# Optimization experiments

Measured on AMD Instinct MI355X. Metric: run time of the kernel, lower is better.

## Reference

```python
import jax, jax.numpy as jnp
import numpy as np

SEQ, B, IN_DIM, EMB, HID, L = 2048, 32, 512, 256, 256, 16
START, STOP = 0, 1
HH = HID // 2  # per-direction hidden size
NEG = -10000.0


def _lstm_dir(xs, Wih, Whh, b, h0, c0, reverse):
    # xs: (T, B, EMB); Wih: (4*HH, EMB); Whh: (4*HH, HH); b: (4*HH,)
    def step(carry, x):
        h, c = carry
        g = x @ Wih.T + h @ Whh.T + b  # (B, 4*HH)
        i, f, gg, o = jnp.split(g, 4, axis=-1)  # PyTorch gate order i,f,g,o
        c = jax.nn.sigmoid(f) * c + jax.nn.sigmoid(i) * jnp.tanh(gg)
        h = jax.nn.sigmoid(o) * jnp.tanh(c)
        return (h, c), h
    _, hs = jax.lax.scan(step, (h0, c0), xs, reverse=reverse)
    return hs  # (T, B, HH)


def _features(source_seq, in_W, in_b, Wih_f, Whh_f, b_f, Wih_b, Whh_b, b_b,
              out_W, out_b, h0, c0):
    x = source_seq @ in_W.T + in_b  # (T, B, EMB)
    hf = _lstm_dir(x, Wih_f, Whh_f, b_f, h0[0], c0[0], reverse=False)
    hb = _lstm_dir(x, Wih_b, Whh_b, b_b, h0[1], c0[1], reverse=True)
    h = jnp.concatenate([hf, hb], axis=-1)  # (T, B, HID)
    return h @ out_W.T + out_b  # (T, B, L)


def _viterbi(feats, transitions):
    # transitions[i, j]: score of transitioning to label i from label j
    fv = jnp.full((B, L), NEG, feats.dtype).at[:, START].set(0.0)

    def step(fv, feat):
        scores = fv[:, None, :] + transitions[None, :, :]  # (B, next, prev)
        bp = jnp.argmax(scores, axis=2).astype(jnp.int32)   # (B, L)
        fv = jnp.max(scores, axis=2) + feat
        return fv, bp

    fv, bps = jax.lax.scan(step, fv, feats)  # bps: (T, B, L)
    term = fv + transitions[STOP][None, :]   # (B, L)
    score = jnp.max(term, axis=1)            # (B,)
    best_last = jnp.argmax(term, axis=1).astype(jnp.int32)  # (B,)

    def back(lbl, bp):
        prev = jnp.take_along_axis(bp, lbl[:, None], axis=1)[:, 0]
        return prev, lbl

    _, path = jax.lax.scan(back, best_last, bps, reverse=True)  # (T, B)
    return score, path


def setup_inputs() -> dict:
    key = jax.random.key(0)
    ks = jax.random.split(key, 16)
    s = 0.05
    return {
        "source_seq": jax.random.normal(ks[0], (SEQ, B, IN_DIM), jnp.float32),
        "in_W": jax.random.normal(ks[1], (EMB, IN_DIM), jnp.float32) * s,
        "in_b": jnp.zeros((EMB,), jnp.float32),
        "Wih_f": jax.random.normal(ks[2], (4 * HH, EMB), jnp.float32) * s,
        "Whh_f": jax.random.normal(ks[3], (4 * HH, HH), jnp.float32) * s,
        "b_f": jnp.zeros((4 * HH,), jnp.float32),
        "Wih_b": jax.random.normal(ks[4], (4 * HH, EMB), jnp.float32) * s,
        "Whh_b": jax.random.normal(ks[5], (4 * HH, HH), jnp.float32) * s,
        "b_b": jnp.zeros((4 * HH,), jnp.float32),
        "out_W": jax.random.normal(ks[6], (L, HID), jnp.float32) * s,
        "out_b": jnp.zeros((L,), jnp.float32),
        "transitions": jax.random.normal(ks[7], (L, L), jnp.float32),
        "h0": jax.random.normal(ks[8], (2, B, HH), jnp.float32),
        "c0": jax.random.normal(ks[9], (2, B, HH), jnp.float32),
    }


def reference(source_seq, in_W, in_b, Wih_f, Whh_f, b_f, Wih_b, Whh_b, b_b,
              out_W, out_b, transitions, h0, c0):
    feats = _features(source_seq, in_W, in_b, Wih_f, Whh_f, b_f,
                      Wih_b, Whh_b, b_b, out_W, out_b, h0, c0)
    score, labels = _viterbi(feats, transitions)
    return score, labels
```

## Files before the change

kernel.cpp:

```cpp
#include <hip/hip_runtime.h>
#include <hip/hip_bf16.h>

typedef __attribute__((ext_vector_type(8))) short bf16x8;
typedef __attribute__((ext_vector_type(4))) float f32x4;
typedef __attribute__((ext_vector_type(4))) unsigned u32x4;
typedef __attribute__((ext_vector_type(2))) unsigned u32x2;

#define SEQT 2048
#define BATCH 32
#define INDIM 512
#define EMB 256
#define HHX 128
#define LBL 16
#define LOG2E 1.44269504f

__device__ __forceinline__ unsigned short f2bf(float f) {
    unsigned u = __float_as_uint(f);
    u += 0x7FFFu + ((u >> 16) & 1u);
    return (unsigned short)(u >> 16);
}
#define BLO(u) __uint_as_float((u) << 16)
#define BHI(u) __uint_as_float((u) & 0xffff0000u)

__device__ __forceinline__ float cell(float ig, float fg, float gg, float og, float& c) {
    float Ef = __builtin_amdgcn_exp2f(fminf(fg, 30.f));
    float Ei = __builtin_amdgcn_exp2f(fminf(ig, 30.f));
    float Eg = __builtin_amdgcn_exp2f(fminf(gg, 60.f));
    float Eo = __builtin_amdgcn_exp2f(fminf(og, 30.f));
    float pf = 1.f + Ef;
    float t1 = (Eg + 1.f) * (1.f + Ei);
    float num = c * t1 + (Eg - 1.f) * pf;
    float cn = num * __builtin_amdgcn_rcpf(pf * t1);
    c = cn;
    float E2 = __builtin_amdgcn_exp2f(fminf(2.f * LOG2E * cn, 60.f));
    float r3 = __builtin_amdgcn_rcpf((E2 + 1.f) * (1.f + Eo));
    return (E2 - 1.f) * r3;
}

__device__ __forceinline__ int orig_of(int gp) {
    return ((gp >> 4) & 3) * 128 + (gp >> 6) * 16 + (gp & 15);
}
__device__ __forceinline__ float gate_scale(int gp) {
    return (((gp >> 4) & 3) == 2) ? (2.f * LOG2E) : (-LOG2E);
}

__global__ __launch_bounds__(256) void k_prep_wc(
    const float* __restrict__ in_W, const float* __restrict__ in_b,
    const float* __restrict__ Wih_f, const float* __restrict__ b_f,
    const float* __restrict__ Wih_b, const float* __restrict__ b_b,
    unsigned short* __restrict__ Wc, float* __restrict__ bc)
{
    int G0 = blockIdx.x * 8;
    int tid = threadIdx.x;
    __shared__ float wrow[8][EMB];
    for (int e = tid; e < 8 * EMB; e += 256) {
        int r = e >> 8, ee = e & 255;
        int G = G0 + r, dir = G >> 9, gp = G & 511;
        wrow[r][ee] = (dir ? Wih_b : Wih_f)[orig_of(gp) * EMB + ee] * gate_scale(gp);
    }
    __syncthreads();
    for (int k = tid; k < INDIM; k += 256) {
        float acc[8] = {0, 0, 0, 0, 0, 0, 0, 0};
        #pragma unroll 4
        for (int e = 0; e < EMB; ++e) {
            float x = in_W[e * INDIM + k];
            #pragma unroll
            for (int r = 0; r < 8; ++r) acc[r] += wrow[r][e] * x;
        }
        #pragma unroll
        for (int r = 0; r < 8; ++r) Wc[(size_t)(G0 + r) * INDIM + k] = f2bf(acc[r]);
    }
    if (tid < 64) {
        for (int r = 0; r < 8; ++r) {
            float p = 0.f;
            for (int e = tid; e < EMB; e += 64) p += wrow[r][e] * in_b[e];
            for (int off = 32; off; off >>= 1) p += __shfl_xor(p, off);
            if (tid == 0) {
                int G = G0 + r, dir = G >> 9, gp = G & 511;
                bc[G] = (dir ? b_b : b_f)[orig_of(gp)] * gate_scale(gp) + p;
            }
        }
    }
}

__global__ __launch_bounds__(256) void k_prep_misc(
    const float* __restrict__ Whh_f, const float* __restrict__ Whh_b,
    const float* __restrict__ out_W,
    unsigned short* __restrict__ Whh_bf, unsigned short* __restrict__ outW_bf)
{
    int idx = blockIdx.x * 256 + threadIdx.x;
    int stride = gridDim.x * 256;
    for (int i = idx; i < 1024 * HHX; i += stride) {
        int G = i >> 7, k = i & 127;
        int dir = G >> 9, gp = G & 511;
        const float* Whh = dir ? Whh_b : Whh_f;
        Whh_bf[i] = f2bf(Whh[orig_of(gp) * HHX + k] * gate_scale(gp));
    }
    for (int i = idx; i < LBL * 256; i += stride) outW_bf[i] = f2bf(out_W[i]);
}

__global__ __launch_bounds__(512) void k_gemm_p(
    const float* __restrict__ S, const unsigned short* __restrict__ Wc,
    const float* __restrict__ bc, unsigned short* __restrict__ P2)
{
    int m0 = blockIdx.y * 64;
    int n0 = blockIdx.x * 256;
    int tid = threadIdx.x;
    int w = tid >> 6, l = tid & 63;
    int lr = l & 15, lq = l >> 4;
    int wm = w >> 2, wn = w & 3;

    __shared__ __align__(16) unsigned short Alds[64 * 64];
    __shared__ __align__(16) unsigned short Blds[256 * 64];

    const f32x4 fzero = {0.f, 0.f, 0.f, 0.f};
    f32x4 acc[2][4];
    #pragma unroll
    for (int a = 0; a < 2; ++a)
        #pragma unroll
        for (int b = 0; b < 4; ++b) acc[a][b] = fzero;

    for (int kt = 0; kt < 8; ++kt) {
        {
            int r = tid >> 3, c = tid & 7;
            const float* src = S + (size_t)(m0 + r) * INDIM + kt * 64 + c * 8;
            float4 v0 = *(const float4*)src;
            float4 v1 = *(const float4*)(src + 4);
            unsigned g0, g1, g2, g3;
            asm("v_cvt_pk_bf16_f32 %0, %1, %2" : "=v"(g0) : "v"(v0.x), "v"(v0.y));
            asm("v_cvt_pk_bf16_f32 %0, %1, %2" : "=v"(g1) : "v"(v0.z), "v"(v0.w));
            asm("v_cvt_pk_bf16_f32 %0, %1, %2" : "=v"(g2) : "v"(v1.x), "v"(v1.y));
            asm("v_cvt_pk_bf16_f32 %0, %1, %2" : "=v"(g3) : "v"(v1.z), "v"(v1.w));
            u32x4 wv = {g0, g1, g2, g3};
            *(u32x4*)((char*)Alds + r * 128 + ((c * 16) ^ ((r & 7) << 4))) = wv;
        }
        {
            int r = tid >> 1, h = tid & 1;
            const unsigned short* bs = Wc + (size_t)(n0 + r) * INDIM + kt * 64;
            #pragma unroll
            for (int cc = 0; cc < 4; ++cc) {
                int ch = h * 4 + cc;
                bf16x8 v = *(const bf16x8*)(bs + ch * 8);
                *(bf16x8*)((char*)Blds + r * 128 + ((ch * 16) ^ ((r & 7) << 4))) = v;
            }
        }
        __syncthreads();
        bf16x8 af[2][2], bfv[4][2];
        #pragma unroll
        for (int tm = 0; tm < 2; ++tm)
            #pragma unroll
            for (int kk = 0; kk < 2; ++kk) {
                int ra = wm * 32 + tm * 16 + lr;
                af[tm][kk] = *(const bf16x8*)((char*)Alds + ra * 128 + ((kk * 64 + lq * 16) ^ ((ra & 7) << 4)));
            }
        #pragma unroll
        for (int tn = 0; tn < 4; ++tn)
            #pragma unroll
            for (int kk = 0; kk < 2; ++kk) {
                int rb = wn * 64 + tn * 16 + lr;
                bfv[tn][kk] = *(const bf16x8*)((char*)Blds + rb * 128 + ((kk * 64 + lq * 16) ^ ((rb & 7) << 4)));
            }
        #pragma unroll
        for (int tm = 0; tm < 2; ++tm)
            #pragma unroll
            for (int tn = 0; tn < 4; ++tn)
                #pragma unroll
                for (int kk = 0; kk < 2; ++kk)
                    acc[tm][tn] = __builtin_amdgcn_mfma_f32_16x16x32_bf16(af[tm][kk], bfv[tn][kk], acc[tm][tn], 0, 0, 0);
        __syncthreads();
    }
    #pragma unroll
    for (int tn = 0; tn < 4; ++tn) {
        int n = n0 + wn * 64 + tn * 16 + lr;
        float bias = bc[n];
        int dir2 = n >> 9, nn = n & 511;
        int w2 = nn >> 6, q2 = (nn >> 4) & 3, lr2 = nn & 15;
        #pragma unroll
        for (int tm = 0; tm < 2; ++tm) {
            int t = blockIdx.y * 2 + wm;
            int bq2 = tm * 4 + lq;
            size_t fr = ((size_t)(t * 2 + dir2) * 8 + bq2) * 512;
            float f0 = acc[tm][tn][0] + bias, f1 = acc[tm][tn][1] + bias;
            float f2 = acc[tm][tn][2] + bias, f3 = acc[tm][tn][3] + bias;
            unsigned p01, p23;
            asm("v_cvt_pk_bf16_f32 %0, %1, %2" : "=v"(p01) : "v"(f0), "v"(f1));
            asm("v_cvt_pk_bf16_f32 %0, %1, %2" : "=v"(p23) : "v"(f2), "v"(f3));
            P2[(fr + (w2 * 64 + 0 * 16 + lr2)) * 4 + q2] = (unsigned short)p01;
            P2[(fr + (w2 * 64 + 1 * 16 + lr2)) * 4 + q2] = (unsigned short)(p01 >> 16);
            P2[(fr + (w2 * 64 + 2 * 16 + lr2)) * 4 + q2] = (unsigned short)p23;
            P2[(fr + (w2 * 64 + 3 * 16 + lr2)) * 4 + q2] = (unsigned short)(p23 >> 16);
        }
    }
}

__global__ __launch_bounds__(512) void k_lstm(
    const unsigned short* __restrict__ P2, const unsigned short* __restrict__ Whh_bf,
    const float* __restrict__ h0, const float* __restrict__ c0,
    unsigned short* __restrict__ H)
{
    int blk = blockIdx.x;
    int dir = blk >> 3, bq = blk & 7;
    int tid = threadIdx.x;
    int w = tid >> 6, l = tid & 63;
    int lr = l & 15, lq = l >> 4;

    __shared__ __align__(16) unsigned short hbuf[2][16 * 128];
    char* hb = (char*)hbuf;

    bf16x8 bfrag[4][4];
    #pragma unroll
    for (int q = 0; q < 4; ++q)
        #pragma unroll
        for (int ko = 0; ko < 4; ++ko) {
            int row = dir * 512 + w * 64 + q * 16 + lr;
            bfrag[q][ko] = *(const bf16x8*)(Whh_bf + (size_t)row * HHX + ko * 32 + lq * 8);
        }

    int u = w * 16 + lr;
    float cA = c0[(dir * 32 + bq * 4 + lq) * HHX + u];

    for (int e = tid; e < 2048; e += 512) {
        int r = e >> 7, uu = e & 127;
        unsigned short v = 0;
        if ((r & 3) == 0) {
            int b = r >> 2;
            v = f2bf(h0[(dir * 32 + bq * 4 + b) * HHX + uu]);
        }
        int addr = (r * 256 + uu * 2) ^ ((r & 7) << 4);
        *(unsigned short*)(hb + addr) = v;
        *(unsigned short*)(hb + 4096 + addr) = 0;
    }
    __syncthreads();

    const int rd0 = (lr * 256 + 0 * 64 + lq * 16) ^ ((lr & 7) << 4);
    const int rd1 = (lr * 256 + 1 * 64 + lq * 16) ^ ((lr & 7) << 4);
    const int rd2 = (lr * 256 + 2 * 64 + lq * 16) ^ ((lr & 7) << 4);
    const int rd3 = (lr * 256 + 3 * 64 + lq * 16) ^ ((lr & 7) << 4);
    const int rA = lq * 4;
    const int waA = (rA * 256 + u * 2) ^ ((rA & 7) << 4);

    int t0 = dir ? (SEQT - 1) : 0;
    const long long pstep = (dir ? -1LL : 1LL) * (2LL * 8 * 512 * 4);
    const unsigned short* pptr = P2 + (((size_t)(t0 * 2 + dir) * 8 + bq) * 512 + tid) * 4;
    u32x2 pc = *(const u32x2*)pptr;
    pptr += pstep;

    unsigned short* hpA = H + ((size_t)t0 * 32 + bq * 4 + lq) * 256 + dir * 128 + u;
    const long long hstep = (dir ? -1LL : 1LL) * (32 * 256);

#define LBAR() asm volatile("s_waitcnt lgkmcnt(0)\n\ts_barrier" ::: "memory")

#define STEP(CUR, PF) do { \
    bf16x8 af0 = *(const bf16x8*)(hb + (CUR) * 4096 + rd0); \
    bf16x8 af1 = *(const bf16x8*)(hb + (CUR) * 4096 + rd1); \
    bf16x8 af2 = *(const bf16x8*)(hb + (CUR) * 4096 + rd2); \
    bf16x8 af3 = *(const bf16x8*)(hb + (CUR) * 4096 + rd3); \
    u32x2 u0 = pc; \
    if (PF) { pc = *(const u32x2*)pptr; pptr += pstep; } \
    f32x4 a0 = {BLO(u0.x), 0.f, 0.f, 0.f}; \
    f32x4 a1 = {BHI(u0.x), 0.f, 0.f, 0.f}; \
    f32x4 a2 = {BLO(u0.y), 0.f, 0.f, 0.f}; \
    f32x4 a3 = {BHI(u0.y), 0.f, 0.f, 0.f}; \
    a0 = __builtin_amdgcn_mfma_f32_16x16x32_bf16(af0, bfrag[0][0], a0, 0, 0, 0); \
    a0 = __builtin_amdgcn_mfma_f32_16x16x32_bf16(af1, bfrag[0][1], a0, 0, 0, 0); \
    a0 = __builtin_amdgcn_mfma_f32_16x16x32_bf16(af2, bfrag[0][2], a0, 0, 0, 0); \
    a0 = __builtin_amdgcn_mfma_f32_16x16x32_bf16(af3, bfrag[0][3], a0, 0, 0, 0); \
    a1 = __builtin_amdgcn_mfma_f32_16x16x32_bf16(af0, bfrag[1][0], a1, 0, 0, 0); \
    a1 = __builtin_amdgcn_mfma_f32_16x16x32_bf16(af1, bfrag[1][1], a1, 0, 0, 0); \
    a1 = __builtin_amdgcn_mfma_f32_16x16x32_bf16(af2, bfrag[1][2], a1, 0, 0, 0); \
    a1 = __builtin_amdgcn_mfma_f32_16x16x32_bf16(af3, bfrag[1][3], a1, 0, 0, 0); \
    a2 = __builtin_amdgcn_mfma_f32_16x16x32_bf16(af0, bfrag[2][0], a2, 0, 0, 0); \
    a2 = __builtin_amdgcn_mfma_f32_16x16x32_bf16(af1, bfrag[2][1], a2, 0, 0, 0); \
    a2 = __builtin_amdgcn_mfma_f32_16x16x32_bf16(af2, bfrag[2][2], a2, 0, 0, 0); \
    a2 = __builtin_amdgcn_mfma_f32_16x16x32_bf16(af3, bfrag[2][3], a2, 0, 0, 0); \
    a3 = __builtin_amdgcn_mfma_f32_16x16x32_bf16(af0, bfrag[3][0], a3, 0, 0, 0); \
    a3 = __builtin_amdgcn_mfma_f32_16x16x32_bf16(af1, bfrag[3][1], a3, 0, 0, 0); \
    a3 = __builtin_amdgcn_mfma_f32_16x16x32_bf16(af2, bfrag[3][2], a3, 0, 0, 0); \
    a3 = __builtin_amdgcn_mfma_f32_16x16x32_bf16(af3, bfrag[3][3], a3, 0, 0, 0); \
    float hnA = cell(a0[0], a1[0], a2[0], a3[0], cA); \
    unsigned pk; \
    asm("v_cvt_pk_bf16_f32 %0, %1, %2" : "=v"(pk) : "v"(hnA), "v"(hnA)); \
    unsigned short sA = (unsigned short)pk; \
    *(unsigned short*)(hb + (((CUR) ^ 1) * 4096) + waA) = sA; \
    hpA[0] = sA; \
    hpA += hstep; \
    LBAR(); \
} while (0)

    for (int it = 0; it < 1023; ++it) {
        STEP(0, true);
        STEP(1, true);
    }
    STEP(0, true);
    STEP(1, false);
#undef STEP
#undef LBAR
}

__global__ __launch_bounds__(256) void k_feats(
    const unsigned short* __restrict__ H, const unsigned short* __restrict__ outW_bf,
    const float* __restrict__ out_b, float* __restrict__ feats)
{
    int m0 = blockIdx.x * 64;
    int tid = threadIdx.x;
    int w = tid >> 6, l = tid & 63;
    int lr = l & 15, lq = l >> 4;
    __shared__ __align__(16) unsigned short Hl[64 * 256];

    {
        int r = tid >> 2, cb = (tid & 3) * 8;
        #pragma unroll
        for (int cc = 0; cc < 8; ++cc) {
            int c = cb + cc;
            bf16x8 v = *(const bf16x8*)(H + (size_t)(m0 + r) * 256 + c * 8);
            *(bf16x8*)((char*)Hl + r * 512 + ((c * 16) ^ ((r & 7) << 4))) = v;
        }
    }
    bf16x8 bw[8];
    #pragma unroll
    for (int ko = 0; ko < 8; ++ko)
        bw[ko] = *(const bf16x8*)(outW_bf + lr * 256 + ko * 32 + lq * 8);
    __syncthreads();
    int row = w * 16 + lr;
    f32x4 acc = {0.f, 0.f, 0.f, 0.f};
    #pragma unroll
    for (int ko = 0; ko < 8; ++ko) {
        bf16x8 a = *(const bf16x8*)((char*)Hl + row * 512 + ((ko * 64 + lq * 16) ^ ((row & 7) << 4)));
        acc = __builtin_amdgcn_mfma_f32_16x16x32_bf16(a, bw[ko], acc, 0, 0, 0);
    }
    float ob = out_b[lr];
    #pragma unroll
    for (int j = 0; j < 4; ++j) {
        int m = m0 + w * 16 + lq * 4 + j;
        feats[(size_t)m * 16 + lr] = acc[j] + ob;
    }
}

template <int CTRL>
__device__ __forceinline__ float dppf(float x) {
    return __int_as_float(__builtin_amdgcn_update_dpp(0, __float_as_int(x), CTRL, 0xF, 0xF, true));
}
template <int CTRL>
__device__ __forceinline__ int dppi(int x) {
    return __builtin_amdgcn_update_dpp(0, x, CTRL, 0xF, 0xF, true);
}

__global__ __launch_bounds__(64) void k_viterbi(
    const float* __restrict__ feats, const float* __restrict__ trans,
    float* __restrict__ out)
{
    int b = blockIdx.x;
    int l = threadIdx.x;
    int i = l >> 2, s = l & 3;
    __shared__ unsigned char bp[SEQT * 16];
    __shared__ __align__(16) float fch[256 * 16];
    __shared__ unsigned long long bp64[SEQT];

    float tr[4];
    #pragma unroll
    for (int m = 0; m < 4; ++m) tr[m] = trans[i * 16 + s * 4 + m];
    float fvloc[4];
    #pragma unroll
    for (int m = 0; m < 4; ++m) fvloc[m] = (s * 4 + m == 0) ? 0.f : -10000.f;

    int ga[4];
    #pragma unroll
    for (int m = 0; m < 4; ++m) ga[m] = (16 * s + 4 * m) * 4;

    for (int t = 0; t < SEQT; ++t) {
        if ((t & 255) == 0) {
            __syncthreads();
            for (int k = l; k < 256; k += 64) {
                const float4* src = (const float4*)(feats + (size_t)((t + k) * 32 + b) * 16);
                float4 v0 = src[0], v1 = src[1], v2 = src[2], v3 = src[3];
                float4* dst = (float4*)(fch + k * 16);
                dst[0] = v0; dst[1] = v1; dst[2] = v2; dst[3] = v3;
            }
            __syncthreads();
        }
        float best = fvloc[0] + tr[0];
        int bj = s * 4;
        #pragma unroll
        for (int m = 1; m < 4; ++m) {
            float v = fvloc[m] + tr[m];
            if (v > best) { best = v; bj = s * 4 + m; }
        }
        {
            float ov = dppf<0xB1>(best); int oj = dppi<0xB1>(bj);
            bool take = (ov > best) || (ov == best && oj < bj);
            best = take ? ov : best; bj = take ? oj : bj;
        }
        {
            float ov = dppf<0x4E>(best); int oj = dppi<0x4E>(bj);
            bool take = (ov > best) || (ov == best && oj < bj);
            best = take ? ov : best; bj = take ? oj : bj;
        }
        float fvn = best + fch[(t & 255) * 16 + i];
        if (s == 0) bp[t * 16 + i] = (unsigned char)bj;
        #pragma unroll
        for (int m = 0; m < 4; ++m)
            fvloc[m] = __int_as_float(__builtin_amdgcn_ds_bpermute(ga[m], __float_as_int(fvn)));
    }
    float bestS = fvloc[0] + trans[16 + s * 4];
    int bl = s * 4;
    #pragma unroll
    for (int m = 1; m < 4; ++m) {
        float tv = fvloc[m] + trans[16 + s * 4 + m];
        if (tv > bestS) { bestS = tv; bl = s * 4 + m; }
    }
    {
        float ov = dppf<0xB1>(bestS); int oj = dppi<0xB1>(bl);
        bool take = (ov > bestS) || (ov == bestS && oj < bl);
        bestS = take ? ov : bestS; bl = take ? oj : bl;
    }
    {
        float ov = dppf<0x4E>(bestS); int oj = dppi<0x4E>(bl);
        bool take = (ov > bestS) || (ov == bestS && oj < bl);
        bestS = take ? ov : bestS; bl = take ? oj : bl;
    }
    __syncthreads();
    for (int t = l; t < SEQT; t += 64) {
        const uint4* p = (const uint4*)(bp + t * 16);
        uint4 u = *p;
        unsigned n0 = (u.x | (u.x >> 4)) & 0x00FF00FFu; n0 = (n0 | (n0 >> 8)) & 0xFFFFu;
        unsigned n1 = (u.y | (u.y >> 4)) & 0x00FF00FFu; n1 = (n1 | (n1 >> 8)) & 0xFFFFu;
        unsigned n2 = (u.z | (u.z >> 4)) & 0x00FF00FFu; n2 = (n2 | (n2 >> 8)) & 0xFFFFu;
        unsigned n3 = (u.w | (u.w >> 4)) & 0x00FF00FFu; n3 = (n3 | (n3 >> 8)) & 0xFFFFu;
        bp64[t] = (unsigned long long)n0 | ((unsigned long long)n1 << 16)
                | ((unsigned long long)n2 << 32) | ((unsigned long long)n3 << 48);
    }
    __syncthreads();
    if (l == 0) out[b] = bestS;
    int lbl = bl;
    #pragma unroll 8
    for (int t = SEQT - 1; t >= 0; --t) {
        if ((t & 63) == l) out[32 + (size_t)t * 32 + b] = (float)lbl;
        lbl = (int)((bp64[t] >> (lbl * 4)) & 15ull);
    }
}

extern "C" void kernel_launch(void* const* d_in, const int* in_sizes, int n_in,
                              void* d_out, int out_size, void* d_ws, size_t ws_size,
                              hipStream_t stream) {
    const float* source = (const float*)d_in[0];
    const float* in_W  = (const float*)d_in[1];
    const float* in_b  = (const float*)d_in[2];
    const float* Wih_f = (const float*)d_in[3];
    const float* Whh_f = (const float*)d_in[4];
    const float* b_f   = (const float*)d_in[5];
    const float* Wih_b = (const float*)d_in[6];
    const float* Whh_b = (const float*)d_in[7];
    const float* b_b   = (const float*)d_in[8];
    const float* out_W = (const float*)d_in[9];
    const float* out_b = (const float*)d_in[10];
    const float* trans = (const float*)d_in[11];
    const float* h0    = (const float*)d_in[12];
    const float* c0    = (const float*)d_in[13];
    float* out = (float*)d_out;

    char* ws = (char*)d_ws;
    unsigned short* P2      = (unsigned short*)(ws);
    unsigned short* H       = (unsigned short*)(ws + 134217728);
    float*          feats   = (float*)         (ws + 167772160);
    unsigned short* Wc      = (unsigned short*)(ws + 171966464);
    float*          bc      = (float*)         (ws + 173015040);
    unsigned short* Whh_bf  = (unsigned short*)(ws + 173019136);
    unsigned short* outW_bf = (unsigned short*)(ws + 173281280);

    hipLaunchKernelGGL(k_prep_wc, dim3(128), dim3(256), 0, stream,
                       in_W, in_b, Wih_f, b_f, Wih_b, b_b, Wc, bc);
    hipLaunchKernelGGL(k_prep_misc, dim3(256), dim3(256), 0, stream,
                       Whh_f, Whh_b, out_W, Whh_bf, outW_bf);
    hipLaunchKernelGGL(k_gemm_p, dim3(4, 1024), dim3(512), 0, stream,
                       source, Wc, bc, P2);
    hipLaunchKernelGGL(k_lstm, dim3(16), dim3(512), 0, stream,
                       P2, Whh_bf, h0, c0, H);
    hipLaunchKernelGGL(k_feats, dim3(1024), dim3(256), 0, stream,
                       H, outW_bf, out_b, feats);
    hipLaunchKernelGGL(k_viterbi, dim3(32), dim3(64), 0, stream,
                       feats, trans, out);
}
```

Measured before the change: 1.824 ms.

## Stage input-projection epilogue through LDS for coalesced 16-byte stores

The GEMM epilogue used to scatter individual 2-byte bf16 values to P2 in the interleaved layout the LSTM kernel expects. It now packs the results into LDS (reusing the B tile buffer) and writes contiguous 16-byte chunks per thread. The P2 layout and the LSTM kernel's read indexing change together to match. This adds a block barrier and LDS traffic and depends on the bounce layout matching the new per-thread read offsets.

```diff
diff --git a/kernel.cpp b/kernel.cpp
--- a/kernel.cpp
+++ b/kernel.cpp
@@ -169,26 +169,37 @@
                     acc[tm][tn] = __builtin_amdgcn_mfma_f32_16x16x32_bf16(af[tm][kk], bfv[tn][kk], acc[tm][tn], 0, 0, 0);
         __syncthreads();
     }
-    #pragma unroll
-    for (int tn = 0; tn < 4; ++tn) {
-        int n = n0 + wn * 64 + tn * 16 + lr;
-        float bias = bc[n];
-        int dir2 = n >> 9, nn = n & 511;
-        int w2 = nn >> 6, q2 = (nn >> 4) & 3, lr2 = nn & 15;
+    char* bounce = (char*)Blds;
+    {
+        float b4[4];
+        #pragma unroll
+        for (int tn = 0; tn < 4; ++tn) b4[tn] = bc[n0 + wn * 64 + tn * 16 + lr];
+        int wbyte = wn * 512 + lr * 32;
         #pragma unroll
         for (int tm = 0; tm < 2; ++tm) {
-            int t = blockIdx.y * 2 + wm;
-            int bq2 = tm * 4 + lq;
-            size_t fr = ((size_t)(t * 2 + dir2) * 8 + bq2) * 512;
-            float f0 = acc[tm][tn][0] + bias, f1 = acc[tm][tn][1] + bias;
-            float f2 = acc[tm][tn][2] + bias, f3 = acc[tm][tn][3] + bias;
-            unsigned p01, p23;
-            asm("v_cvt_pk_bf16_f32 %0, %1, %2" : "=v"(p01) : "v"(f0), "v"(f1));
-            asm("v_cvt_pk_bf16_f32 %0, %1, %2" : "=v"(p23) : "v"(f2), "v"(f3));
-            P2[(fr + (w2 * 64 + 0 * 16 + lr2)) * 4 + q2] = (unsigned short)p01;
-            P2[(fr + (w2 * 64 + 1 * 16 + lr2)) * 4 + q2] = (unsigned short)(p01 >> 16);
-            P2[(fr + (w2 * 64 + 2 * 16 + lr2)) * 4 + q2] = (unsigned short)p23;
-            P2[(fr + (w2 * 64 + 3 * 16 + lr2)) * 4 + q2] = (unsigned short)(p23 >> 16);
+            #pragma unroll
+            for (int j = 0; j < 4; ++j) {
+                float f0 = acc[tm][0][j] + b4[0], f1 = acc[tm][1][j] + b4[1];
+                float f2 = acc[tm][2][j] + b4[2], f3 = acc[tm][3][j] + b4[3];
+                unsigned pA, pB;
+                asm("v_cvt_pk_bf16_f32 %0, %1, %2" : "=v"(pA) : "v"(f0), "v"(f1));
+                asm("v_cvt_pk_bf16_f32 %0, %1, %2" : "=v"(pB) : "v"(f2), "v"(f3));
+                *(u32x2*)(bounce + (wm * 8 + tm * 4 + lq) * 2048 + wbyte + j * 8) = (u32x2){pA, pB};
+            }
+        }
+    }
+    __syncthreads();
+    {
+        int dirg = blockIdx.x >> 1;
+        int halfoff = (blockIdx.x & 1) * 2048;
+        #pragma unroll
+        for (int s = 0; s < 4; ++s) {
+            int idx = tid * 4 + s;
+            int fl = idx >> 7, infr = (idx & 127) * 16;
+            int t = blockIdx.y * 2 + (fl >> 3), bq = fl & 7;
+            u32x4 v = *(u32x4*)(bounce + idx * 16);
+            char* dst = (char*)P2 + ((size_t)((t * 2 + dirg) * 8 + bq)) * 4096 + halfoff + infr;
+            *(u32x4*)dst = v;
         }
     }
 }
@@ -240,8 +251,8 @@
     const int waA = (rA * 256 + u * 2) ^ ((rA & 7) << 4);
 
     int t0 = dir ? (SEQT - 1) : 0;
-    const long long pstep = (dir ? -1LL : 1LL) * (2LL * 8 * 512 * 4);
-    const unsigned short* pptr = P2 + (((size_t)(t0 * 2 + dir) * 8 + bq) * 512 + tid) * 4;
+    const long long pstep = (dir ? -1LL : 1LL) * (2LL * 8 * 2048);
+    const unsigned short* pptr = P2 + ((size_t)(t0 * 2 + dir) * 8 + bq) * 2048 + ((size_t)u * 4 + lq) * 4;
     u32x2 pc = *(const u32x2*)pptr;
     pptr += pstep;
 
```

Result: no change. 1.832 ms (+0.4%).
